# Optimization experiments

Measured on AMD Instinct MI355X. Metric: run time of the kernel, lower is better.

Reference implementation:

```python
import jax, jax.numpy as jnp
import numpy as np

D = 256; H = 8; DH = D // H; FF = 1024; L = 2048; M = 1024


def _mlp(x, w0, b0, w1, b1, w2, b2):
    # 3-layer MLP, relu on all but last (matches MLP class)
    x = jax.nn.relu(x @ w0 + b0)
    x = jax.nn.relu(x @ w1 + b1)
    return x @ w2 + b2


def _ln(x, g, b, eps=1e-5):
    m = jnp.mean(x, axis=-1, keepdims=True)
    v = jnp.var(x, axis=-1, keepdims=True)
    return (x - m) * jax.lax.rsqrt(v + eps) * g + b


def setup_inputs():
    key = jax.random.key(0)
    ks = jax.random.split(key, 16)
    p = lambda i, shape: jax.random.normal(ks[i], shape, jnp.float32) * 0.02
    z = lambda *s: jnp.zeros(s, jnp.float32)
    o = lambda *s: jnp.ones(s, jnp.float32)
    # positions: ego covers [0, L), agent covers [L-M, 2L-M) -> exactly M shared positions
    return {
        'ego_q': jax.random.normal(ks[0], (1, L, D), jnp.float32),
        'agent_q': jax.random.normal(ks[1], (1, L, D), jnp.float32),
        'ego_pos': jnp.arange(L, dtype=jnp.int32),
        'agent_pos': jnp.arange(L, dtype=jnp.int32) + (L - M),
        'n_match': M,
        'fw0': p(2, (2 * D, D)), 'fb0': z(D),
        'fw1': p(3, (D, D)), 'fb1': z(D),
        'fw2': p(4, (D, D)), 'fb2': z(D),
        'wq': p(5, (D, D)), 'bq': z(D),
        'wk': p(6, (D, D)), 'bk': z(D),
        'wv': p(7, (D, D)), 'bv': z(D),
        'wo': p(8, (D, D)), 'bo': z(D),
        'g1': o(D), 'be1': z(D),
        'l1w': p(9, (D, FF)), 'l1b': z(FF),
        'l2w': p(10, (FF, D)), 'l2b': z(D),
        'g2': o(D), 'be2': z(D),
    }


def reference(ego_q, agent_q, ego_pos, agent_pos, n_match,
              fw0, fb0, fw1, fb1, fw2, fb2,
              wq, bq, wk, bk, wv, bv, wo, bo,
              g1, be1, l1w, l1b, l2w, l2b, g2, be2):
    La = agent_pos.shape[0]
    # vectorized replacement of the per-position dict/loop grouping:
    # for each ego position, find a matching agent position (positions sorted+unique)
    idx = jnp.clip(jnp.searchsorted(agent_pos, ego_pos), 0, La - 1)
    matched = (agent_pos[idx] == ego_pos)                     # (L,)
    pair = jnp.concatenate([ego_q, agent_q[:, idx, :]], axis=-1)  # (1, L, 2D)
    fused = _mlp(pair, fw0, fb0, fw1, fb1, fw2, fb2)          # (1, L, D)
    ego_out = jnp.where(matched[None, :, None], fused, ego_q)
    # agent queries whose positions are NOT in ego's set: indices [n_match, La)
    q = jnp.concatenate([ego_out, agent_q[:, n_match:, :]], axis=1)  # (1, 2L-M, D)
    kv = jnp.concatenate([ego_q, agent_q], axis=1)                   # (1, 2L, D)
    # MultiheadAttention (batch_first, eval mode -> no dropout)
    qh = (q @ wq + bq).reshape(1, -1, H, DH)
    kh = (kv @ wk + bk).reshape(1, -1, H, DH)
    vh = (kv @ wv + bv).reshape(1, -1, H, DH)
    scores = jnp.einsum('bqhd,bkhd->bhqk', qh, kh) * (1.0 / np.sqrt(DH))
    attn = jax.nn.softmax(scores, axis=-1)
    o = jnp.einsum('bhqk,bkhd->bqhd', attn, vh).reshape(1, -1, D) @ wo + bo
    x = _ln(q + o, g1, be1)
    ff = jax.nn.relu(x @ l1w + l1b) @ l2w + l2b
    return _ln(x + ff, g2, be2)
```

## Files before the change

kernel.cpp:

```cpp
#include <hip/hip_runtime.h>
#include <hip/hip_bf16.h>

typedef __hip_bfloat16 bf16;
typedef __bf16 bf16x8 __attribute__((ext_vector_type(8)));
typedef float  f32x16 __attribute__((ext_vector_type(16)));

__device__ __forceinline__ bool is_bf16_flag(const unsigned* g1w) {
    return *g1w == 0x3F803F80u;
}

__device__ __forceinline__ unsigned cvt_pk_bf16(float lo, float hi) {
    unsigned w;
    asm("v_cvt_pk_bf16_f32 %0, %1, %2" : "=v"(w) : "v"(lo), "v"(hi));
    return w;
}
__device__ __forceinline__ void permlane32_swap(unsigned& a, unsigned& b) {
    asm("v_permlane32_swap_b32 %0, %1" : "+v"(a), "+v"(b));
}

union FragU { unsigned u[4]; uint4 q; bf16x8 v; };

__device__ __forceinline__ float loadf(const void* p, size_t i, bool isb) {
    return isb ? __bfloat162float(((const bf16*)p)[i]) : ((const float*)p)[i];
}

__device__ __forceinline__ float4 load4rt(const void* p, size_t i, bool isb) {
    if (isb) {
        uint2 u = *(const uint2*)((const bf16*)p + i);
        float4 f;
        f.x = __uint_as_float(u.x << 16);
        f.y = __uint_as_float(u.x & 0xFFFF0000u);
        f.z = __uint_as_float(u.y << 16);
        f.w = __uint_as_float(u.y & 0xFFFF0000u);
        return f;
    }
    return *(const float4*)((const float*)p + i);
}

__device__ __forceinline__ void store4b(bf16* p, float4 v) {
    uint2 w;
    w.x = cvt_pk_bf16(v.x, v.y);
    w.y = cvt_pk_bf16(v.z, v.w);
    *(uint2*)p = w;
}

__device__ __forceinline__ float4 load4b(const bf16* p) {
    uint2 u = *(const uint2*)p;
    float4 f;
    f.x = __uint_as_float(u.x << 16);
    f.y = __uint_as_float(u.x & 0xFFFF0000u);
    f.z = __uint_as_float(u.y << 16);
    f.w = __uint_as_float(u.y & 0xFFFF0000u);
    return f;
}

#define NCVT 13
#define NWT 9
struct PreArgs {
    const void* csrc[NCVT];
    float*      cdst[NCVT];
    float       cscale[NCVT];
    int         cn4[NCVT];
    int         cblk_end[NCVT];
    int         cvt_blocks;
    const void* wsrc[NWT];
    bf16*       wdst[NWT];
    int         wK[NWT];
    int         wN[NWT];
    float       wscale[NWT];
    int         wblk_end[NWT];
    int         wt_blocks;
    const void* ego; const void* agent;
    const int*  epos; const int* apos;
    int         La;
    bf16*       pair;
    int*        mflag;
};

__global__ void preprocess_kernel(PreArgs a, const unsigned* __restrict__ g1w) {
    bool isb = is_bf16_flag(g1w);
    __shared__ float ld[64][65];
    __shared__ int s_idx[2];
    int b = blockIdx.x;
    int tid = threadIdx.x;
    if (b < a.cvt_blocks) {
        int t = 0;
        while (b >= a.cblk_end[t]) t++;
        int base = (t == 0) ? 0 : a.cblk_end[t - 1];
        int i = (b - base) * 256 + tid;
        if (i >= a.cn4[t]) return;
        float sc = a.cscale[t];
        float4 r = load4rt(a.csrc[t], (size_t)i * 4, isb);
        r.x *= sc; r.y *= sc; r.z *= sc; r.w *= sc;
        ((float4*)a.cdst[t])[i] = r;
    } else if (b < a.cvt_blocks + a.wt_blocks) {
        b -= a.cvt_blocks;
        int w = 0;
        while (b >= a.wblk_end[w]) w++;
        int base = (w == 0) ? 0 : a.wblk_end[w - 1];
        int tt = b - base;
        int tn = a.wN[w] >> 6;
        int kr = (tt / tn) * 64, nc = (tt % tn) * 64;
        int N = a.wN[w], K = a.wK[w];
        float sc = a.wscale[w];
        const void* src = a.wsrc[w];
#pragma unroll
        for (int i = 0; i < 16; i++) {
            int f = tid + i * 256;
            int r = f >> 6, c = f & 63;
            ld[r][c] = loadf(src, (size_t)(kr + r) * N + nc + c, isb) * sc;
        }
        __syncthreads();
        bf16* dst = a.wdst[w];
#pragma unroll
        for (int i = 0; i < 16; i++) {
            int f = tid + i * 256;
            int c = f >> 6, r = f & 63;
            dst[(size_t)(nc + c) * K + kr + r] = __float2bfloat16(ld[r][c]);
        }
    } else {
        b -= a.cvt_blocks + a.wt_blocks;
        int rb = tid >> 7;
        int row = b * 2 + rb;
        int cc = (tid & 127) * 4;
        if ((tid & 127) == 0) {
            int p = a.epos[row];
            int lo = 0, hi = a.La;
            while (lo < hi) { int mid = (lo + hi) >> 1; if (a.apos[mid] < p) lo = mid + 1; else hi = mid; }
            int idx = lo < a.La - 1 ? lo : a.La - 1;
            s_idx[rb] = idx;
            a.mflag[row] = (a.apos[idx] == p) ? 1 : 0;
        }
        __syncthreads();
        int idx = s_idx[rb];
        float4 v = (cc < 256) ? load4rt(a.ego, (size_t)row * 256 + cc, isb)
                              : load4rt(a.agent, (size_t)idx * 256 + (cc - 256), isb);
        store4b(a.pair + (size_t)row * 512 + cc, v);
    }
}

template<int RELU>
__device__ __forceinline__ void gemm_core(const bf16* __restrict__ A, const bf16* __restrict__ Bt,
                                          const float* __restrict__ bias, bf16* __restrict__ C,
                                          int K, int lda, int ldb, int ldc,
                                          int bm, int bn, bool addBias,
                                          char* sA, char* sB) {
    const int t = threadIdx.x;
    const int lane = t & 63, wave = t >> 6;
    const int hi = lane >> 5, ql = lane & 31;
    const int wm = (wave & 1) * 32, wn = (wave >> 1) * 32;

    const int r0 = t >> 3, ch0 = t & 7;
    const int r1 = 32 + r0;
    const int wb0 = (r0 * 128 + ch0 * 16) ^ ((r0 & 7) << 4);
    const int wb1 = (r1 * 128 + ch0 * 16) ^ ((r1 & 7) << 4);

    uint4 ra0, ra1, rb0, rb1;
    ra0 = *(const uint4*)&A [(size_t)(bm + r0) * lda + ch0 * 8];
    ra1 = *(const uint4*)&A [(size_t)(bm + r1) * lda + ch0 * 8];
    rb0 = *(const uint4*)&Bt[(size_t)(bn + r0) * ldb + ch0 * 8];
    rb1 = *(const uint4*)&Bt[(size_t)(bn + r1) * ldb + ch0 * 8];

    f32x16 acc = {};
    const int swzA = ((wm + ql) & 7) << 4;
    const int swzB = ((wn + ql) & 7) << 4;
    const int rowA = (wm + ql) * 128;
    const int rowB = (wn + ql) * 128;

    for (int k0 = 0; k0 < K; k0 += 64) {
        __syncthreads();
        *(uint4*)(sA + wb0) = ra0;
        *(uint4*)(sA + wb1) = ra1;
        *(uint4*)(sB + wb0) = rb0;
        *(uint4*)(sB + wb1) = rb1;
        if (k0 + 64 < K) {
            int kn = k0 + 64;
            ra0 = *(const uint4*)&A [(size_t)(bm + r0) * lda + kn + ch0 * 8];
            ra1 = *(const uint4*)&A [(size_t)(bm + r1) * lda + kn + ch0 * 8];
            rb0 = *(const uint4*)&Bt[(size_t)(bn + r0) * ldb + kn + ch0 * 8];
            rb1 = *(const uint4*)&Bt[(size_t)(bn + r1) * ldb + kn + ch0 * 8];
        }
        __syncthreads();
#pragma unroll
        for (int kc = 0; kc < 4; kc++) {
            FragU af, bf_;
            af.q  = *(const uint4*)(sA + ((rowA + kc * 32 + hi * 16) ^ swzA));
            bf_.q = *(const uint4*)(sB + ((rowB + kc * 32 + hi * 16) ^ swzB));
            acc = __builtin_amdgcn_mfma_f32_32x32x16_bf16(af.v, bf_.v, acc, 0, 0, 0);
        }
    }

    int gn = bn + wn + ql;
    float bsv = addBias ? bias[gn] : 0.f;
#pragma unroll
    for (int r = 0; r < 16; r++) {
        int mrow = (r & 3) + 8 * (r >> 2) + 4 * hi;
        float v = acc[r] + bsv;
        if (RELU) v = fmaxf(v, 0.f);
        C[(size_t)(bm + wm + mrow) * ldc + gn] = __float2bfloat16(v);
    }
}

template<int RELU>
__launch_bounds__(256)
__global__ void gemm_bf16_kernel(const bf16* __restrict__ A, const bf16* __restrict__ Bt,
                                 const float* __restrict__ bias, bf16* __restrict__ C,
                                 int M, int N, int K, int lda, int ldb, int ldc) {
    __shared__ __align__(16) char sA[64 * 128];
    __shared__ __align__(16) char sB[64 * 128];
    const int z = blockIdx.z;
    gemm_core<RELU>(A + (size_t)z * K, Bt + (size_t)z * K, bias, C + (size_t)z * M * ldc,
                    K, lda, ldb, ldc, blockIdx.y * 64, blockIdx.x * 64, z == 0, sA, sB);
}

struct GemmP {
    const bf16* A; const bf16* Bt; const float* bias; bf16* C;
    int K, lda, ldb, ldc, nx;
};

__launch_bounds__(256)
__global__ void gemm_dual_kernel(GemmP p0, GemmP p1, int nblk0) {
    __shared__ __align__(16) char sA[64 * 128];
    __shared__ __align__(16) char sB[64 * 128];
    int b = blockIdx.x;
    const GemmP& p = (b < nblk0) ? p0 : p1;
    int t = (b < nblk0) ? b : b - nblk0;
    int bn = (t % p.nx) * 64, bm = (t / p.nx) * 64;
    gemm_core<0>(p.A, p.Bt, p.bias, p.C, p.K, p.lda, p.ldb, p.ldc, bm, bn, true, sA, sB);
}

__global__ void build_qkv_kernel(const void* __restrict__ ego, const void* __restrict__ agent,
                                 const bf16* __restrict__ fused, const int* __restrict__ mflag,
                                 int L, int Mm, int Nq, int Nk,
                                 bf16* __restrict__ qb, bf16* __restrict__ kvb,
                                 const unsigned* __restrict__ g1w) {
    bool isb = is_bf16_flag(g1w);
    int wave = threadIdx.x >> 6, lane = threadIdx.x & 63;
    int r = blockIdx.x * 4 + wave;
    int col = lane * 4;
    float4 kvv = (r < L) ? load4rt(ego, (size_t)r * 256 + col, isb)
                         : load4rt(agent, (size_t)(r - L) * 256 + col, isb);
    store4b(kvb + (size_t)r * 256 + col, kvv);
    if (r < Nq) {
        float4 qv;
        if (r < L) qv = mflag[r] ? load4b(fused + (size_t)r * 256 + col)
                                 : load4rt(ego, (size_t)r * 256 + col, isb);
        else       qv = load4rt(agent, (size_t)(Mm + r - L) * 256 + col, isb);
        store4b(qb + (size_t)r * 256 + col, qv);
    }
}

#define SPLITS 8

__launch_bounds__(256)
__global__ void attn_mfma_kernel(const bf16* __restrict__ qh,
                                 const bf16* __restrict__ kvh,
                                 float* __restrict__ pm, float* __restrict__ pl,
                                 bf16* __restrict__ pacc,
                                 int Nq, int Nk) {
    __shared__ __align__(16) char sK[2][64 * 128];
    __shared__ __align__(16) char sV[2][32 * 128];

    const int h = blockIdx.y, z = blockIdx.z;
    const int t = threadIdx.x;
    const int wave = t >> 6, lane = t & 63;
    const int ql = lane & 31, hi = lane >> 5;
    const int qbase = blockIdx.x * 128 + wave * 32;
    const int kbeg = z * (Nk / SPLITS);
    const int nkk = Nk / SPLITS;

    FragU qf0, qf1;
    {
        const bf16* qp = qh + (size_t)(qbase + ql) * 256 + h * 32;
        qf0.q = *(const uint4*)(qp + hi * 8);
        qf1.q = *(const uint4*)(qp + 16 + hi * 8);
    }

    float mrun = -1e30f, lrun = 0.f;
    f32x16 acc = {};

    const int skey = t >> 2, sch = t & 3;
    const int kwb = (skey * 128 + sch * 16) ^ ((skey & 7) << 4);

    uint4 rk = *(const uint4*)(kvh + (size_t)(kbeg + skey) * 512 + h * 32 + sch * 8);
    uint4 rv = *(const uint4*)(kvh + (size_t)(kbeg + lane) * 512 + 256 + h * 32 + wave * 8);

    int cur = 0;
#pragma unroll 1
    for (int t0 = 0; t0 < nkk; t0 += 64) {
        char* sKc = sK[cur];
        char* sVc = sV[cur];
        *(uint4*)(sKc + kwb) = rk;
        {
            unsigned short sv[8] = {
                (unsigned short)(rv.x), (unsigned short)(rv.x >> 16),
                (unsigned short)(rv.y), (unsigned short)(rv.y >> 16),
                (unsigned short)(rv.z), (unsigned short)(rv.z >> 16),
                (unsigned short)(rv.w), (unsigned short)(rv.w >> 16)};
#pragma unroll
            for (int i = 0; i < 8; i++) {
                int dh = wave * 8 + i;
                *(unsigned short*)(sVc + dh * 128 + ((lane * 2) ^ (i << 4))) = sv[i];
            }
        }
        if (t0 + 64 < nkk) {
            rk = *(const uint4*)(kvh + (size_t)(kbeg + t0 + 64 + skey) * 512 + h * 32 + sch * 8);
            rv = *(const uint4*)(kvh + (size_t)(kbeg + t0 + 64 + lane) * 512 + 256 + h * 32 + wave * 8);
        }
        __syncthreads();

        FragU ka, kb;
        f32x16 s0 = {}, s1 = {};
        {
            int row0 = ql, row1 = 32 + ql;
            int swzk = (ql & 7) << 4;
            ka.q = *(const uint4*)(sKc + ((row0 * 128 + hi * 16) ^ swzk));
            s0 = __builtin_amdgcn_mfma_f32_32x32x16_bf16(ka.v, qf0.v, s0, 0, 0, 0);
            ka.q = *(const uint4*)(sKc + ((row0 * 128 + 32 + hi * 16) ^ swzk));
            s0 = __builtin_amdgcn_mfma_f32_32x32x16_bf16(ka.v, qf1.v, s0, 0, 0, 0);
            kb.q = *(const uint4*)(sKc + ((row1 * 128 + hi * 16) ^ swzk));
            s1 = __builtin_amdgcn_mfma_f32_32x32x16_bf16(kb.v, qf0.v, s1, 0, 0, 0);
            kb.q = *(const uint4*)(sKc + ((row1 * 128 + 32 + hi * 16) ^ swzk));
            s1 = __builtin_amdgcn_mfma_f32_32x32x16_bf16(kb.v, qf1.v, s1, 0, 0, 0);
        }

        float tm = -1e30f;
#pragma unroll
        for (int r = 0; r < 16; r++) tm = fmaxf(tm, fmaxf(s0[r], s1[r]));
        tm = fmaxf(tm, __shfl_xor(tm, 32));
        if (!__all(tm <= mrun)) {
            float mn = fmaxf(mrun, tm);
            float cf = __builtin_amdgcn_exp2f(mrun - mn);
            mrun = mn;
#pragma unroll
            for (int r = 0; r < 16; r++) acc[r] *= cf;
            lrun *= cf;
        }

        float p0[16], p1[16];
        float ls = 0.f;
#pragma unroll
        for (int r = 0; r < 16; r++) { p0[r] = __builtin_amdgcn_exp2f(s0[r] - mrun); ls += p0[r]; }
#pragma unroll
        for (int r = 0; r < 16; r++) { p1[r] = __builtin_amdgcn_exp2f(s1[r] - mrun); ls += p1[r]; }
        ls += __shfl_xor(ls, 32);
        lrun += ls;

        int swzk = (ql & 7) << 4;
        FragU vf, pa;
        {
            unsigned a = cvt_pk_bf16(p0[0], p0[1]),  b = cvt_pk_bf16(p0[2], p0[3]);
            unsigned c = cvt_pk_bf16(p0[4], p0[5]),  d = cvt_pk_bf16(p0[6], p0[7]);
            permlane32_swap(a, c); permlane32_swap(b, d);
            pa.u[0] = a; pa.u[1] = b; pa.u[2] = c; pa.u[3] = d;
            vf.q = *(const uint4*)(sVc + ((ql * 128 + hi * 16) ^ swzk));
            acc = __builtin_amdgcn_mfma_f32_32x32x16_bf16(vf.v, pa.v, acc, 0, 0, 0);
            unsigned e = cvt_pk_bf16(p0[8], p0[9]),   f = cvt_pk_bf16(p0[10], p0[11]);
            unsigned g = cvt_pk_bf16(p0[12], p0[13]), h2 = cvt_pk_bf16(p0[14], p0[15]);
            permlane32_swap(e, g); permlane32_swap(f, h2);
            pa.u[0] = e; pa.u[1] = f; pa.u[2] = g; pa.u[3] = h2;
            vf.q = *(const uint4*)(sVc + ((ql * 128 + 32 + hi * 16) ^ swzk));
            acc = __builtin_amdgcn_mfma_f32_32x32x16_bf16(vf.v, pa.v, acc, 0, 0, 0);
        }
        {
            unsigned a = cvt_pk_bf16(p1[0], p1[1]),  b = cvt_pk_bf16(p1[2], p1[3]);
            unsigned c = cvt_pk_bf16(p1[4], p1[5]),  d = cvt_pk_bf16(p1[6], p1[7]);
            permlane32_swap(a, c); permlane32_swap(b, d);
            pa.u[0] = a; pa.u[1] = b; pa.u[2] = c; pa.u[3] = d;
            vf.q = *(const uint4*)(sVc + ((ql * 128 + 64 + hi * 16) ^ swzk));
            acc = __builtin_amdgcn_mfma_f32_32x32x16_bf16(vf.v, pa.v, acc, 0, 0, 0);
            unsigned e = cvt_pk_bf16(p1[8], p1[9]),   f = cvt_pk_bf16(p1[10], p1[11]);
            unsigned g = cvt_pk_bf16(p1[12], p1[13]), h2 = cvt_pk_bf16(p1[14], p1[15]);
            permlane32_swap(e, g); permlane32_swap(f, h2);
            pa.u[0] = e; pa.u[1] = f; pa.u[2] = g; pa.u[3] = h2;
            vf.q = *(const uint4*)(sVc + ((ql * 128 + 96 + hi * 16) ^ swzk));
            acc = __builtin_amdgcn_mfma_f32_32x32x16_bf16(vf.v, pa.v, acc, 0, 0, 0);
        }
        cur ^= 1;
    }

    if (hi == 0) {
        pm[((size_t)z * 8 + h) * Nq + qbase + ql] = mrun;
        pl[((size_t)z * 8 + h) * Nq + qbase + ql] = lrun;
    }
#pragma unroll
    for (int r = 0; r < 16; r++) {
        int dh = (r & 3) + 8 * (r >> 2) + 4 * hi;
        pacc[(((size_t)z * 8 + h) * 32 + dh) * (size_t)Nq + qbase + ql] = __float2bfloat16(acc[r]);
    }
}

__global__ void attn_merge_kernel(const float* __restrict__ pm, const float* __restrict__ pl,
                                  const bf16* __restrict__ pacc, bf16* __restrict__ o, int Nq) {
    int q = blockIdx.x * 256 + threadIdx.x;
    int h = blockIdx.y, dg = blockIdx.z;
    float ml[SPLITS];
    float M = -1e30f;
#pragma unroll
    for (int s = 0; s < SPLITS; s++) {
        ml[s] = pm[((size_t)s * 8 + h) * Nq + q];
        M = fmaxf(M, ml[s]);
    }
    float L = 0.f;
    float w[SPLITS];
#pragma unroll
    for (int s = 0; s < SPLITS; s++) {
        w[s] = __builtin_amdgcn_exp2f(ml[s] - M);
        L += pl[((size_t)s * 8 + h) * Nq + q] * w[s];
    }
    float inv = 1.f / L;
#pragma unroll
    for (int j = 0; j < 4; j++) {
        int d = dg * 4 + j;
        float a = 0.f;
#pragma unroll
        for (int s = 0; s < SPLITS; s++)
            a += __bfloat162float(pacc[(((size_t)s * 8 + h) * 32 + d) * (size_t)Nq + q]) * w[s];
        o[(size_t)q * 256 + h * 32 + d] = __float2bfloat16(a * inv);
    }
}

__global__ void ln_kernel(const bf16* __restrict__ a, const bf16* __restrict__ b,
                          const bf16* __restrict__ c,
                          const float* __restrict__ g, const float* __restrict__ be,
                          bf16* __restrict__ outf16, void* __restrict__ outb,
                          const unsigned* __restrict__ g1w) {
    int wave = threadIdx.x >> 6, lane = threadIdx.x & 63;
    int row = blockIdx.x * 4 + wave;
    int col = lane * 4;
    size_t base = (size_t)row * 256 + col;
    float4 av = load4b(a + base);
    float4 bv = load4b(b + base);
    float x0 = av.x + bv.x, x1 = av.y + bv.y, x2 = av.z + bv.z, x3 = av.w + bv.w;
    if (c) {
        float4 cv = load4b(c + base);
        x0 += cv.x; x1 += cv.y; x2 += cv.z; x3 += cv.w;
    }
    float s  = x0 + x1 + x2 + x3;
    float s2 = x0 * x0 + x1 * x1 + x2 * x2 + x3 * x3;
#pragma unroll
    for (int off = 32; off; off >>= 1) { s += __shfl_xor(s, off); s2 += __shfl_xor(s2, off); }
    float mean = s * (1.f / 256.f);
    float var  = s2 * (1.f / 256.f) - mean * mean;
    float rs = rsqrtf(var + 1e-5f);
    float4 gv = *(const float4*)(g + col);
    float4 bev = *(const float4*)(be + col);
    float y0 = (x0 - mean) * rs * gv.x + bev.x;
    float y1 = (x1 - mean) * rs * gv.y + bev.y;
    float y2 = (x2 - mean) * rs * gv.z + bev.z;
    float y3 = (x3 - mean) * rs * gv.w + bev.w;
    if (outf16) {
        store4b(outf16 + base, make_float4(y0, y1, y2, y3));
    } else if (is_bf16_flag(g1w)) {
        store4b((bf16*)outb + base, make_float4(y0, y1, y2, y3));
    } else {
        *(float4*)((float*)outb + base) = make_float4(y0, y1, y2, y3);
    }
}

extern "C" void kernel_launch(void* const* d_in, const int* in_sizes, int n_in,
                              void* d_out, int out_size, void* d_ws, size_t ws_size,
                              hipStream_t stream) {
    const int Dd = 256;
    const int L  = in_sizes[2];
    const int La = in_sizes[3];
    const int Nk = L + La;
    const int Nq = out_size / Dd;
    const int Mm = L + La - Nq;
    const float scale = 0.17677669529663687f * 1.4426950408889634f;

    const unsigned* g1w = (const unsigned*)d_in[19];

    float* W = (float*)d_ws;
    size_t off = 0;
    auto alloc = [&](size_t n) { size_t o = off; off += n; return o; };
    (void)ws_size; (void)n_in;

    size_t o_fb0 = alloc(256), o_fb1 = alloc(256), o_fb2 = alloc(256);
    size_t o_bq = alloc(256), o_bkv = alloc(512), o_bo = alloc(256);
    size_t o_g1 = alloc(256), o_be1 = alloc(256);
    size_t o_l1b = alloc(1024), o_l2b = alloc(256);
    size_t o_g2 = alloc(256), o_be2 = alloc(256);

    size_t o_fw0t = alloc(65536), o_fw1t = alloc(32768), o_fw2t = alloc(32768);
    size_t o_wqt = alloc(32768), o_wkvt = alloc(65536), o_wot = alloc(32768);
    size_t o_l1wt = alloc(131072), o_l2wt = alloc(131072);
    size_t o_pair = alloc((size_t)L * 256);
    size_t o_h1 = alloc((size_t)L * 128), o_h2 = alloc((size_t)L * 128);
    size_t o_fused = alloc((size_t)L * 128);
    size_t o_q   = alloc((size_t)Nq * 128);
    size_t o_kv  = alloc((size_t)Nk * 128);
    size_t o_qh  = alloc((size_t)Nq * 128);
    size_t o_kvh = alloc((size_t)Nk * 256);
    size_t o_ao  = alloc((size_t)Nq * 128);
    size_t o_opp = alloc((size_t)Nq * 256);
    size_t o_x   = alloc((size_t)Nq * 128);
    size_t o_ff1 = alloc((size_t)Nq * 512);
    size_t o_ff2p = alloc((size_t)Nq * 256);
    size_t o_pacc = alloc((size_t)SPLITS * 8 * 16 * Nq);
    size_t o_pm   = alloc((size_t)SPLITS * 8 * Nq);
    size_t o_pl   = alloc((size_t)SPLITS * 8 * Nq);
    size_t o_ints = alloc((size_t)L);
    int* mflag = (int*)(W + o_ints);

    auto B16 = [&](size_t o) { return (bf16*)(W + o); };

    {
        PreArgs pa;
        const int csrcs[NCVT] = {6, 8, 10, 12, 14, 16, 18, 19, 20, 22, 24, 25, 26};
        const size_t cdsts[NCVT] = {o_fb0, o_fb1, o_fb2, o_bq, o_bkv, o_bkv + 256, o_bo,
                                    o_g1, o_be1, o_l1b, o_l2b, o_g2, o_be2};
        int blk = 0;
        for (int i = 0; i < NCVT; i++) {
            pa.csrc[i] = d_in[csrcs[i]];
            pa.cdst[i] = W + cdsts[i];
            pa.cscale[i] = (csrcs[i] == 12) ? scale : 1.0f;
            pa.cn4[i] = in_sizes[csrcs[i]] / 4;
            blk += (pa.cn4[i] + 255) / 256;
            pa.cblk_end[i] = blk;
        }
        pa.cvt_blocks = blk;

        const int wsrcs[NWT] = {5, 7, 9, 11, 13, 15, 17, 21, 23};
        bf16* wdsts[NWT] = {B16(o_fw0t), B16(o_fw1t), B16(o_fw2t), B16(o_wqt),
                            B16(o_wkvt), B16(o_wkvt) + 65536, B16(o_wot),
                            B16(o_l1wt), B16(o_l2wt)};
        const int Ks[NWT] = {512, 256, 256, 256, 256, 256, 256, 256, 1024};
        const int Ns[NWT] = {256, 256, 256, 256, 256, 256, 256, 1024, 256};
        int wblk = 0;
        for (int i = 0; i < NWT; i++) {
            pa.wsrc[i] = d_in[wsrcs[i]];
            pa.wdst[i] = wdsts[i];
            pa.wK[i] = Ks[i]; pa.wN[i] = Ns[i];
            pa.wscale[i] = (wsrcs[i] == 11) ? scale : 1.0f;
            wblk += (Ks[i] / 64) * (Ns[i] / 64);
            pa.wblk_end[i] = wblk;
        }
        pa.wt_blocks = wblk;

        pa.ego = d_in[0]; pa.agent = d_in[1];
        pa.epos = (const int*)d_in[2]; pa.apos = (const int*)d_in[3];
        pa.La = La; pa.pair = B16(o_pair); pa.mflag = mflag;

        int total = pa.cvt_blocks + pa.wt_blocks + L / 2;
        preprocess_kernel<<<total, 256, 0, stream>>>(pa, g1w);
    }

    gemm_bf16_kernel<1><<<dim3(4, L/64), 256, 0, stream>>>(B16(o_pair), B16(o_fw0t), W + o_fb0, B16(o_h1),    L, 256, 512, 512, 512, 256);
    gemm_bf16_kernel<1><<<dim3(4, L/64), 256, 0, stream>>>(B16(o_h1),   B16(o_fw1t), W + o_fb1, B16(o_h2),    L, 256, 256, 256, 256, 256);
    gemm_bf16_kernel<0><<<dim3(4, L/64), 256, 0, stream>>>(B16(o_h2),   B16(o_fw2t), W + o_fb2, B16(o_fused), L, 256, 256, 256, 256, 256);

    build_qkv_kernel<<<Nk / 4, 256, 0, stream>>>(d_in[0], d_in[1], B16(o_fused), mflag,
                                                 L, Mm, Nq, Nk, B16(o_q), B16(o_kv), g1w);

    {
        GemmP p0{B16(o_q),  B16(o_wqt),  W + o_bq,  B16(o_qh),  256, 256, 256, 256, 4};
        GemmP p1{B16(o_kv), B16(o_wkvt), W + o_bkv, B16(o_kvh), 256, 256, 256, 512, 8};
        int nblk0 = 4 * (Nq / 64);
        int nblk1 = 8 * (Nk / 64);
        gemm_dual_kernel<<<nblk0 + nblk1, 256, 0, stream>>>(p0, p1, nblk0);
    }

    attn_mfma_kernel<<<dim3(Nq/128, 8, SPLITS), 256, 0, stream>>>(B16(o_qh), B16(o_kvh),
                                                                  W + o_pm, W + o_pl, B16(o_pacc),
                                                                  Nq, Nk);
    attn_merge_kernel<<<dim3(Nq/256, 8, 8), 256, 0, stream>>>(W + o_pm, W + o_pl, B16(o_pacc),
                                                              B16(o_ao), Nq);

    gemm_bf16_kernel<0><<<dim3(4, Nq/64, 2), 256, 0, stream>>>(B16(o_ao), B16(o_wot), W + o_bo, B16(o_opp), Nq, 256, 128, 256, 256, 256);
    ln_kernel<<<Nq / 4, 256, 0, stream>>>(B16(o_q), B16(o_opp), B16(o_opp) + (size_t)Nq * 256,
                                          W + o_g1, W + o_be1, B16(o_x), nullptr, g1w);

    gemm_bf16_kernel<1><<<dim3(16, Nq/64), 256, 0, stream>>>(B16(o_x),   B16(o_l1wt), W + o_l1b, B16(o_ff1), Nq, 1024, 256, 256, 256, 1024);
    gemm_bf16_kernel<0><<<dim3(4,  Nq/64, 2), 256, 0, stream>>>(B16(o_ff1), B16(o_l2wt), W + o_l2b, B16(o_ff2p), Nq, 256, 512, 1024, 1024, 256);
    ln_kernel<<<Nq / 4, 256, 0, stream>>>(B16(o_x), B16(o_ff2p), B16(o_ff2p) + (size_t)Nq * 256,
                                          W + o_g2, W + o_be2, nullptr, d_out, g1w);
}
```

Before: 97.76 us.

## Move KV build into preprocess and co-schedule KV projection with first MLP layer

The KV concat/convert is moved into the preprocess kernel, since it does not depend on the MLP. The KV projection GEMM now runs in the same launch as the first MLP GEMM, which is independent of it, instead of alongside the Q projection. The Q projection becomes its own launch after the MLP. This fills the GPU better during the small MLP GEMMs, at the cost of one extra launch for the Q GEMM.

Result: no change. 96.51 us (-1.3%).

```diff
diff --git a/kernel.cpp b/kernel.cpp
--- a/kernel.cpp
+++ b/kernel.cpp
@@ -72,9 +72,11 @@
     int         wt_blocks;
     const void* ego; const void* agent;
     const int*  epos; const int* apos;
-    int         La;
+    int         La; int L;
     bf16*       pair;
     int*        mflag;
+    int         pair_blocks;
+    bf16*       kvb;
 };
 
 __global__ void preprocess_kernel(PreArgs a, const unsigned* __restrict__ g1w) {
@@ -118,7 +120,7 @@
             int c = f >> 6, r = f & 63;
             dst[(size_t)(nc + c) * K + kr + r] = __float2bfloat16(ld[r][c]);
         }
-    } else {
+    } else if (b < a.cvt_blocks + a.wt_blocks + a.pair_blocks) {
         b -= a.cvt_blocks + a.wt_blocks;
         int rb = tid >> 7;
         int row = b * 2 + rb;
@@ -136,6 +138,14 @@
         float4 v = (cc < 256) ? load4rt(a.ego, (size_t)row * 256 + cc, isb)
                               : load4rt(a.agent, (size_t)idx * 256 + (cc - 256), isb);
         store4b(a.pair + (size_t)row * 512 + cc, v);
+    } else {
+        b -= a.cvt_blocks + a.wt_blocks + a.pair_blocks;
+        int wave = tid >> 6, lane = tid & 63;
+        int r = b * 4 + wave;
+        int col = lane * 4;
+        float4 kvv = (r < a.L) ? load4rt(a.ego, (size_t)r * 256 + col, isb)
+                               : load4rt(a.agent, (size_t)(r - a.L) * 256 + col, isb);
+        store4b(a.kvb + (size_t)r * 256 + col, kvv);
     }
 }
 
@@ -218,36 +228,36 @@
     int K, lda, ldb, ldc, nx;
 };
 
+template<int R0, int R1>
 __launch_bounds__(256)
 __global__ void gemm_dual_kernel(GemmP p0, GemmP p1, int nblk0) {
     __shared__ __align__(16) char sA[64 * 128];
     __shared__ __align__(16) char sB[64 * 128];
     int b = blockIdx.x;
-    const GemmP& p = (b < nblk0) ? p0 : p1;
-    int t = (b < nblk0) ? b : b - nblk0;
-    int bn = (t % p.nx) * 64, bm = (t / p.nx) * 64;
-    gemm_core<0>(p.A, p.Bt, p.bias, p.C, p.K, p.lda, p.ldb, p.ldc, bm, bn, true, sA, sB);
-}
-
-__global__ void build_qkv_kernel(const void* __restrict__ ego, const void* __restrict__ agent,
-                                 const bf16* __restrict__ fused, const int* __restrict__ mflag,
-                                 int L, int Mm, int Nq, int Nk,
-                                 bf16* __restrict__ qb, bf16* __restrict__ kvb,
-                                 const unsigned* __restrict__ g1w) {
+    if (b < nblk0) {
+        int bn = (b % p0.nx) * 64, bm = (b / p0.nx) * 64;
+        gemm_core<R0>(p0.A, p0.Bt, p0.bias, p0.C, p0.K, p0.lda, p0.ldb, p0.ldc, bm, bn, true, sA, sB);
+    } else {
+        b -= nblk0;
+        int bn = (b % p1.nx) * 64, bm = (b / p1.nx) * 64;
+        gemm_core<R1>(p1.A, p1.Bt, p1.bias, p1.C, p1.K, p1.lda, p1.ldb, p1.ldc, bm, bn, true, sA, sB);
+    }
+}
+
+__global__ void build_q_kernel(const void* __restrict__ ego, const void* __restrict__ agent,
+                               const bf16* __restrict__ fused, const int* __restrict__ mflag,
+                               int L, int Mm, int Nq,
+                               bf16* __restrict__ qb,
+                               const unsigned* __restrict__ g1w) {
     bool isb = is_bf16_flag(g1w);
     int wave = threadIdx.x >> 6, lane = threadIdx.x & 63;
     int r = blockIdx.x * 4 + wave;
     int col = lane * 4;
-    float4 kvv = (r < L) ? load4rt(ego, (size_t)r * 256 + col, isb)
-                         : load4rt(agent, (size_t)(r - L) * 256 + col, isb);
-    store4b(kvb + (size_t)r * 256 + col, kvv);
-    if (r < Nq) {
-        float4 qv;
-        if (r < L) qv = mflag[r] ? load4b(fused + (size_t)r * 256 + col)
-                                 : load4rt(ego, (size_t)r * 256 + col, isb);
-        else       qv = load4rt(agent, (size_t)(Mm + r - L) * 256 + col, isb);
-        store4b(qb + (size_t)r * 256 + col, qv);
-    }
+    float4 qv;
+    if (r < L) qv = mflag[r] ? load4b(fused + (size_t)r * 256 + col)
+                             : load4rt(ego, (size_t)r * 256 + col, isb);
+    else       qv = load4rt(agent, (size_t)(Mm + r - L) * 256 + col, isb);
+    store4b(qb + (size_t)r * 256 + col, qv);
 }
 
 #define SPLITS 8
@@ -540,26 +550,29 @@
 
         pa.ego = d_in[0]; pa.agent = d_in[1];
         pa.epos = (const int*)d_in[2]; pa.apos = (const int*)d_in[3];
-        pa.La = La; pa.pair = B16(o_pair); pa.mflag = mflag;
-
-        int total = pa.cvt_blocks + pa.wt_blocks + L / 2;
+        pa.La = La; pa.L = L;
+        pa.pair = B16(o_pair); pa.mflag = mflag;
+        pa.pair_blocks = L / 2;
+        pa.kvb = B16(o_kv);
+
+        int total = pa.cvt_blocks + pa.wt_blocks + pa.pair_blocks + Nk / 4;
         preprocess_kernel<<<total, 256, 0, stream>>>(pa, g1w);
     }
 
-    gemm_bf16_kernel<1><<<dim3(4, L/64), 256, 0, stream>>>(B16(o_pair), B16(o_fw0t), W + o_fb0, B16(o_h1),    L, 256, 512, 512, 512, 256);
-    gemm_bf16_kernel<1><<<dim3(4, L/64), 256, 0, stream>>>(B16(o_h1),   B16(o_fw1t), W + o_fb1, B16(o_h2),    L, 256, 256, 256, 256, 256);
-    gemm_bf16_kernel<0><<<dim3(4, L/64), 256, 0, stream>>>(B16(o_h2),   B16(o_fw2t), W + o_fb2, B16(o_fused), L, 256, 256, 256, 256, 256);
-
-    build_qkv_kernel<<<Nk / 4, 256, 0, stream>>>(d_in[0], d_in[1], B16(o_fused), mflag,
-                                                 L, Mm, Nq, Nk, B16(o_q), B16(o_kv), g1w);
-
     {
-        GemmP p0{B16(o_q),  B16(o_wqt),  W + o_bq,  B16(o_qh),  256, 256, 256, 256, 4};
-        GemmP p1{B16(o_kv), B16(o_wkvt), W + o_bkv, B16(o_kvh), 256, 256, 256, 512, 8};
-        int nblk0 = 4 * (Nq / 64);
+        GemmP p0{B16(o_pair), B16(o_fw0t), W + o_fb0, B16(o_h1),  512, 512, 512, 256, 4};
+        GemmP p1{B16(o_kv),   B16(o_wkvt), W + o_bkv, B16(o_kvh), 256, 256, 256, 512, 8};
+        int nblk0 = 4 * (L / 64);
         int nblk1 = 8 * (Nk / 64);
-        gemm_dual_kernel<<<nblk0 + nblk1, 256, 0, stream>>>(p0, p1, nblk0);
-    }
+        gemm_dual_kernel<1, 0><<<nblk0 + nblk1, 256, 0, stream>>>(p0, p1, nblk0);
+    }
+
+    gemm_bf16_kernel<1><<<dim3(4, L/64), 256, 0, stream>>>(B16(o_h1), B16(o_fw1t), W + o_fb1, B16(o_h2),    L, 256, 256, 256, 256, 256);
+    gemm_bf16_kernel<0><<<dim3(4, L/64), 256, 0, stream>>>(B16(o_h2), B16(o_fw2t), W + o_fb2, B16(o_fused), L, 256, 256, 256, 256, 256);
+
+    build_q_kernel<<<Nq / 4, 256, 0, stream>>>(d_in[0], d_in[1], B16(o_fused), mflag,
+                                               L, Mm, Nq, B16(o_q), g1w);
+    gemm_bf16_kernel<0><<<dim3(4, Nq/64), 256, 0, stream>>>(B16(o_q), B16(o_wqt), W + o_bq, B16(o_qh), Nq, 256, 256, 256, 256, 256);
 
     attn_mfma_kernel<<<dim3(Nq/128, 8, SPLITS), 256, 0, stream>>>(B16(o_qh), B16(o_kvh),
                                                                   W + o_pm, W + o_pl, B16(o_pacc),
```
